# Performance work log

Hardware: AMD Instinct MI355X
Metric: run time of the kernel (lower is better)

The kernel has to match this reference:

```python
import jax, jax.numpy as jnp
import numpy as np

N, M, D = 16384, 2048, 512


def setup_inputs() -> dict:
    key = jax.random.key(0)
    k1, k2 = jax.random.split(key)
    x = jax.random.normal(k1, (N, D), dtype=jnp.float32)
    centers = jax.random.normal(k2, (M, D), dtype=jnp.float32)
    log_sigmas = jnp.zeros((M,), dtype=jnp.float32)
    return {"x": x, "centers": centers, "log_sigmas": log_sigmas}


def reference(x, centers, log_sigmas):
    x_sq = jnp.sum(x * x, axis=1, keepdims=True)          # [N, 1]
    c_sq = jnp.sum(centers * centers, axis=1)             # [M]
    cross = jnp.einsum("nd,md->nm", x, centers)           # [N, M] GEMM
    d = x_sq + c_sq[None, :] - 2.0 * cross                # [N, M]
    sigmas = jnp.exp(log_sigmas)                          # [M]
    return jnp.exp(-d / (2.0 * sigmas[None, :] ** 2))     # [N, M]
```

## Files before the change

kernel.cpp:

```cpp
#include <hip/hip_runtime.h>
#include <hip/hip_bf16.h>
#include <stdint.h>

#define N_ROWS 16384
#define M_COLS 2048
#define D_DIM  512

typedef __attribute__((ext_vector_type(4))) float f32x4;
typedef __attribute__((ext_vector_type(2))) int   i32x2;
typedef long i64;

#define AS1 __attribute__((address_space(1)))
#define AS3 __attribute__((address_space(3)))

__global__ __launch_bounds__(256) void conv_all(const float* __restrict__ x,
                                                const float* __restrict__ cen,
                                                const float* __restrict__ ls,
                                                unsigned char* __restrict__ xb,
                                                unsigned char* __restrict__ cb,
                                                float* __restrict__ xsq,
                                                float* __restrict__ csq,
                                                float* __restrict__ nsc) {
  const int gr   = blockIdx.x * 4 + (threadIdx.x >> 6);
  const int lane = threadIdx.x & 63;
  const float* src;
  unsigned char* dst;
  float* sq;
  int row;
  bool is_c = (gr >= N_ROWS);
  if (is_c) { row = gr - N_ROWS; src = cen; dst = cb; sq = csq; }
  else      { row = gr;          src = x;   dst = xb; sq = xsq; }

  const float* s = src + (size_t)row * D_DIM + lane * 8;
  f32x4 v0 = *(const f32x4*)s;
  f32x4 v1 = *(const f32x4*)(s + 4);
  float acc = v0.x*v0.x + v0.y*v0.y + v0.z*v0.z + v0.w*v0.w
            + v1.x*v1.x + v1.y*v1.y + v1.z*v1.z + v1.w*v1.w;
  i32x2 o;
  int w0 = __builtin_amdgcn_cvt_pk_fp8_f32(v0.x, v0.y, 0, false);
  w0     = __builtin_amdgcn_cvt_pk_fp8_f32(v0.z, v0.w, w0, true);
  int w1 = __builtin_amdgcn_cvt_pk_fp8_f32(v1.x, v1.y, 0, false);
  w1     = __builtin_amdgcn_cvt_pk_fp8_f32(v1.z, v1.w, w1, true);
  o[0] = w0; o[1] = w1;
  *(i32x2*)(dst + (size_t)row * D_DIM + lane * 8) = o;
  #pragma unroll
  for (int off = 32; off > 0; off >>= 1) acc += __shfl_down(acc, off, 64);
  if (lane == 0) sq[row] = acc;
  if (is_c && lane == 1) nsc[row] = -0.5f * expf(-2.0f * ls[row]);
}

static __device__ __forceinline__ void gl2lds16(const unsigned char* g, unsigned char* l) {
  __builtin_amdgcn_global_load_lds((const AS1 uint32_t*)g, (AS3 uint32_t*)l, 16, 0, 0);
}

__global__ __launch_bounds__(256) void gemm_rbf(const unsigned char* __restrict__ A8,
                                                const unsigned char* __restrict__ B8,
                                                const float* __restrict__ xsq,
                                                const float* __restrict__ csq,
                                                const float* __restrict__ nscale,
                                                float* __restrict__ out) {
  __shared__ unsigned char As[128 * 128];
  __shared__ unsigned char Bs[128 * 128];

  const int t    = threadIdx.x;
  const int lane = t & 63;
  const int w    = t >> 6;
  const int wr   = w >> 1, wc = w & 1;
  const int rowBase = blockIdx.y * 128;
  const int colBase = blockIdx.x * 128;

  const int lrow = t >> 3;
  const int lkc  = ((t & 7) ^ ((t >> 3) & 7)) * 16;

  const unsigned char* aG = A8 + (size_t)(rowBase + lrow) * D_DIM + lkc;
  const unsigned char* bG = B8 + (size_t)(colBase + lrow) * D_DIM + lkc;
  unsigned char* aL = &As[t * 16];
  unsigned char* bL = &Bs[t * 16];

  f32x4 acc[4][4];
  #pragma unroll
  for (int i = 0; i < 4; ++i)
    #pragma unroll
    for (int j = 0; j < 4; ++j)
      #pragma unroll
      for (int r = 0; r < 4; ++r) acc[i][j][r] = 0.0f;

  const int fr  = lane & 15;
  const int q16 = lane >> 4;
  const int sw  = fr & 7;
  const int sub = (q16 & 1) * 8;

  for (int kt = 0; kt < D_DIM; kt += 128) {
    __syncthreads();
    #pragma unroll
    for (int q = 0; q < 4; ++q) {
      gl2lds16(aG + kt + (size_t)(q * 32) * D_DIM, aL + q * 4096);
      gl2lds16(bG + kt + (size_t)(q * 32) * D_DIM, bL + q * 4096);
    }
    __syncthreads();

    #pragma unroll
    for (int ks = 0; ks < 4; ++ks) {
      const int pc = ((ks * 2 + (q16 >> 1)) ^ sw) * 16 + sub;
      i64 af[4], bfr[4];
      #pragma unroll
      for (int i = 0; i < 4; ++i)
        af[i] = *(const i64*)&As[(wr * 64 + i * 16 + fr) * 128 + pc];
      #pragma unroll
      for (int j = 0; j < 4; ++j)
        bfr[j] = *(const i64*)&Bs[(wc * 64 + j * 16 + fr) * 128 + pc];

      #pragma unroll
      for (int i = 0; i < 4; ++i)
        #pragma unroll
        for (int j = 0; j < 4; ++j)
          acc[i][j] = __builtin_amdgcn_mfma_f32_16x16x32_fp8_fp8(af[i], bfr[j], acc[i][j], 0, 0, 0);
    }
  }

  const int rq = q16 * 4;
  float xs[4][4];
  #pragma unroll
  for (int i = 0; i < 4; ++i)
    #pragma unroll
    for (int r = 0; r < 4; ++r)
      xs[i][r] = xsq[rowBase + wr * 64 + i * 16 + rq + r];

  #pragma unroll
  for (int j = 0; j < 4; ++j) {
    const int c    = colBase + wc * 64 + j * 16 + fr;
    const float cs  = csq[c];
    const float nsc = nscale[c];
    #pragma unroll
    for (int i = 0; i < 4; ++i) {
      const int r0 = rowBase + wr * 64 + i * 16 + rq;
      #pragma unroll
      for (int r = 0; r < 4; ++r) {
        const float dv = xs[i][r] + cs - 2.0f * acc[i][j][r];
        out[(size_t)(r0 + r) * M_COLS + c] = __expf(dv * nsc);
      }
    }
  }
}

__global__ __launch_bounds__(256) void rbf_fallback(const float* __restrict__ x,
                                                    const float* __restrict__ cen,
                                                    const float* __restrict__ ls,
                                                    float* __restrict__ out) {
  __shared__ float xr[D_DIM];
  const int n = blockIdx.y;
  const int m = blockIdx.x * 256 + threadIdx.x;
  for (int d = threadIdx.x; d < D_DIM; d += 256) xr[d] = x[(size_t)n * D_DIM + d];
  __syncthreads();
  const float* cp = cen + (size_t)m * D_DIM;
  float acc = 0.f;
  for (int d = 0; d < D_DIM; d += 4) {
    f32x4 cv = *(const f32x4*)(cp + d);
    float d0 = xr[d + 0] - cv.x;
    float d1 = xr[d + 1] - cv.y;
    float d2 = xr[d + 2] - cv.z;
    float d3 = xr[d + 3] - cv.w;
    acc += d0 * d0 + d1 * d1 + d2 * d2 + d3 * d3;
  }
  const float nsc = -0.5f * expf(-2.0f * ls[m]);
  out[(size_t)n * M_COLS + m] = __expf(acc * nsc);
}

extern "C" void kernel_launch(void* const* d_in, const int* in_sizes, int n_in,
                              void* d_out, int out_size, void* d_ws, size_t ws_size,
                              hipStream_t stream) {
  const float* x   = (const float*)d_in[0];
  const float* cen = (const float*)d_in[1];
  const float* ls  = (const float*)d_in[2];
  float* out = (float*)d_out;

  const size_t need = (size_t)N_ROWS * D_DIM
                    + (size_t)M_COLS * D_DIM
                    + (size_t)N_ROWS * 4
                    + (size_t)M_COLS * 4
                    + (size_t)M_COLS * 4;

  if (ws_size >= need) {
    char* p = (char*)d_ws;
    unsigned char* xb = (unsigned char*)p; p += (size_t)N_ROWS * D_DIM;
    unsigned char* cb = (unsigned char*)p; p += (size_t)M_COLS * D_DIM;
    float* xsq   = (float*)p; p += (size_t)N_ROWS * 4;
    float* csq   = (float*)p; p += (size_t)M_COLS * 4;
    float* nsc   = (float*)p;

    conv_all<<<(N_ROWS + M_COLS) / 4, 256, 0, stream>>>(x, cen, ls, xb, cb, xsq, csq, nsc);
    dim3 grid(M_COLS / 128, N_ROWS / 128);
    gemm_rbf<<<grid, 256, 0, stream>>>(xb, cb, xsq, csq, nsc, out);
  } else {
    dim3 grid(M_COLS / 256, N_ROWS);
    rbf_fallback<<<grid, 256, 0, stream>>>(x, cen, ls, out);
  }
}
```

Before: 177.4 us.

## Double-buffer LDS K-tiles in fp8 GEMM and use nontemporal output stores

```diff
diff --git a/kernel.cpp b/kernel.cpp
--- a/kernel.cpp
+++ b/kernel.cpp
@@ -59,8 +59,8 @@
                                                 const float* __restrict__ csq,
                                                 const float* __restrict__ nscale,
                                                 float* __restrict__ out) {
-  __shared__ unsigned char As[128 * 128];
-  __shared__ unsigned char Bs[128 * 128];
+  __shared__ unsigned char As0[64 * 128], Bs0[64 * 128];
+  __shared__ unsigned char As1[64 * 128], Bs1[64 * 128];
 
   const int t    = threadIdx.x;
   const int lane = t & 63;
@@ -69,13 +69,18 @@
   const int rowBase = blockIdx.y * 128;
   const int colBase = blockIdx.x * 128;
 
-  const int lrow = t >> 3;
-  const int lkc  = ((t & 7) ^ ((t >> 3) & 7)) * 16;
-
-  const unsigned char* aG = A8 + (size_t)(rowBase + lrow) * D_DIM + lkc;
-  const unsigned char* bG = B8 + (size_t)(colBase + lrow) * D_DIM + lkc;
-  unsigned char* aL = &As[t * 16];
-  unsigned char* bL = &Bs[t * 16];
+  int aOff[2], bOff[2];
+  #pragma unroll
+  for (int q = 0; q < 2; ++q) {
+    const int s    = q * 256 + t;
+    const int mr   = s >> 3;
+    const int c8   = (s & 7) ^ (mr & 7);
+    const int srow = 2 * mr + (c8 >> 2);
+    const int skc  = (c8 & 3) * 16;
+    aOff[q] = (rowBase + srow) * D_DIM + skc;
+    bOff[q] = (colBase + srow) * D_DIM + skc;
+  }
+  const int ld0 = t * 16, ld1 = 4096 + t * 16;
 
   f32x4 acc[4][4];
   #pragma unroll
@@ -87,36 +92,54 @@
 
   const int fr  = lane & 15;
   const int q16 = lane >> 4;
-  const int sw  = fr & 7;
+  const int frh = fr >> 1;
+  const int c4  = (fr & 1) * 4;
+  const int khi = q16 >> 1;
   const int sub = (q16 & 1) * 8;
-
-  for (int kt = 0; kt < D_DIM; kt += 128) {
+  const int arB = (wr * 32 + frh) * 128;
+  const int brB = (wc * 32 + frh) * 128;
+
+#define STAGE(Ab, Bb, kt) do {                      \
+    gl2lds16(A8 + aOff[0] + (kt), (Ab) + ld0);      \
+    gl2lds16(A8 + aOff[1] + (kt), (Ab) + ld1);      \
+    gl2lds16(B8 + bOff[0] + (kt), (Bb) + ld0);      \
+    gl2lds16(B8 + bOff[1] + (kt), (Bb) + ld1);      \
+  } while (0)
+
+#define COMPUTE(Ab, Bb) do {                                                  \
+    _Pragma("unroll")                                                         \
+    for (int ks = 0; ks < 2; ++ks) {                                          \
+      const int pc = ((c4 + ks * 2 + khi) ^ frh) * 16 + sub;                  \
+      i64 af[4], bfr[4];                                                      \
+      _Pragma("unroll")                                                       \
+      for (int i = 0; i < 4; ++i)                                             \
+        af[i] = *(const i64*)&(Ab)[arB + i * 1024 + pc];                      \
+      _Pragma("unroll")                                                       \
+      for (int j = 0; j < 4; ++j)                                             \
+        bfr[j] = *(const i64*)&(Bb)[brB + j * 1024 + pc];                     \
+      _Pragma("unroll")                                                       \
+      for (int i = 0; i < 4; ++i)                                             \
+        _Pragma("unroll")                                                     \
+        for (int j = 0; j < 4; ++j)                                           \
+          acc[i][j] = __builtin_amdgcn_mfma_f32_16x16x32_fp8_fp8(             \
+              af[i], bfr[j], acc[i][j], 0, 0, 0);                             \
+    }                                                                         \
+  } while (0)
+
+  STAGE(As0, Bs0, 0);
+  __syncthreads();
+  #pragma unroll
+  for (int kk = 0; kk < 4; ++kk) {
+    STAGE(As1, Bs1, kk * 128 + 64);
+    COMPUTE(As0, Bs0);
     __syncthreads();
-    #pragma unroll
-    for (int q = 0; q < 4; ++q) {
-      gl2lds16(aG + kt + (size_t)(q * 32) * D_DIM, aL + q * 4096);
-      gl2lds16(bG + kt + (size_t)(q * 32) * D_DIM, bL + q * 4096);
-    }
-    __syncthreads();
-
-    #pragma unroll
-    for (int ks = 0; ks < 4; ++ks) {
-      const int pc = ((ks * 2 + (q16 >> 1)) ^ sw) * 16 + sub;
-      i64 af[4], bfr[4];
-      #pragma unroll
-      for (int i = 0; i < 4; ++i)
-        af[i] = *(const i64*)&As[(wr * 64 + i * 16 + fr) * 128 + pc];
-      #pragma unroll
-      for (int j = 0; j < 4; ++j)
-        bfr[j] = *(const i64*)&Bs[(wc * 64 + j * 16 + fr) * 128 + pc];
-
-      #pragma unroll
-      for (int i = 0; i < 4; ++i)
-        #pragma unroll
-        for (int j = 0; j < 4; ++j)
-          acc[i][j] = __builtin_amdgcn_mfma_f32_16x16x32_fp8_fp8(af[i], bfr[j], acc[i][j], 0, 0, 0);
-    }
-  }
+    if (kk < 3) STAGE(As0, Bs0, kk * 128 + 128);
+    COMPUTE(As1, Bs1);
+    if (kk < 3) __syncthreads();
+  }
+
+#undef STAGE
+#undef COMPUTE
 
   const int rq = q16 * 4;
   float xs[4][4];
@@ -128,7 +151,7 @@
 
   #pragma unroll
   for (int j = 0; j < 4; ++j) {
-    const int c    = colBase + wc * 64 + j * 16 + fr;
+    const int c     = colBase + wc * 64 + j * 16 + fr;
     const float cs  = csq[c];
     const float nsc = nscale[c];
     #pragma unroll
@@ -137,7 +160,8 @@
       #pragma unroll
       for (int r = 0; r < 4; ++r) {
         const float dv = xs[i][r] + cs - 2.0f * acc[i][j][r];
-        out[(size_t)(r0 + r) * M_COLS + c] = __expf(dv * nsc);
+        __builtin_nontemporal_store(__expf(dv * nsc),
+                                    &out[(size_t)(r0 + r) * M_COLS + c]);
       }
     }
   }
```

New measurement: 180.7 us. No clear change (+1.9%).
